# Performance work log

Measured on AMD Instinct MI355X. Metric: run time of the kernel, lower is better.

## Reference

```python
import jax, jax.numpy as jnp
import numpy as np

N, K, D = 65536, 1024, 512
ALPHA = 1.0

def setup_inputs() -> dict:
    key = jax.random.key(0)
    k1, k2 = jax.random.split(key)
    batch = jax.random.normal(k1, (N, D), dtype=jnp.float32)
    # Xavier uniform init for cluster centers: bound = sqrt(6/(K+D))
    bound = float(np.sqrt(6.0 / (K + D)))
    cluster_centers = jax.random.uniform(k2, (K, D), dtype=jnp.float32, minval=-bound, maxval=bound)
    return {"batch": batch, "cluster_centers": cluster_centers}

def reference(batch, cluster_centers):
    x_sq = jnp.sum(batch * batch, axis=1, keepdims=True)            # [N,1]
    c_sq = jnp.sum(cluster_centers * cluster_centers, axis=1)       # [K]
    cross = batch @ cluster_centers.T                               # [N,K]
    norm_squared = jnp.maximum(x_sq - 2.0 * cross + c_sq[None, :], 0.0)
    numerator = 1.0 / (1.0 + norm_squared / ALPHA)
    power = (ALPHA + 1.0) / 2.0
    numerator = numerator ** power
    return numerator / jnp.sum(numerator, axis=1, keepdims=True)
```

## Files before the change

kernel.cpp:

```cpp
#include <hip/hip_runtime.h>
#include <hip/hip_bf16.h>
#include <stdint.h>


#define N_ROWS 65536
#define K_CL   1024
#define D_DIM  512
#define BM     64

typedef __attribute__((ext_vector_type(8))) short short8;
typedef __attribute__((ext_vector_type(4))) float f32x4;

__device__ __forceinline__ ushort f2bf(float f) {
    union { float f; uint32_t u; } v; v.f = f;
    uint32_t u = v.u;
    u += 0x7fffu + ((u >> 16) & 1u);
    return (ushort)(u >> 16);
}

__device__ __forceinline__ float waveReduceSum(float s) {
#pragma unroll
    for (int off = 32; off; off >>= 1) s += __shfl_down(s, off, 64);
    return s;
}

__global__ void prep_rows(const float* __restrict__ X, ushort* __restrict__ Xbf,
                          float* __restrict__ sq) {
    const int row  = blockIdx.x * 4 + (threadIdx.x >> 6);
    const int lane = threadIdx.x & 63;
    const float4* src = (const float4*)(X + (size_t)row * D_DIM);
    float4 a = src[lane * 2];
    float4 b = src[lane * 2 + 1];
    float s = (a.x*a.x + a.y*a.y) + (a.z*a.z + a.w*a.w)
            + (b.x*b.x + b.y*b.y) + (b.z*b.z + b.w*b.w);
    uint4 o;
    o.x = (uint32_t)f2bf(a.x) | ((uint32_t)f2bf(a.y) << 16);
    o.y = (uint32_t)f2bf(a.z) | ((uint32_t)f2bf(a.w) << 16);
    o.z = (uint32_t)f2bf(b.x) | ((uint32_t)f2bf(b.y) << 16);
    o.w = (uint32_t)f2bf(b.z) | ((uint32_t)f2bf(b.w) << 16);
    *(uint4*)(Xbf + (size_t)row * D_DIM + lane * 8) = o;
    s = waveReduceSum(s);
    if (lane == 0) sq[row] = s;
}

__global__ __launch_bounds__(512, 2) void gemm_fused(
    const ushort* __restrict__ A, const ushort* __restrict__ B,
    const float* __restrict__ xsq, const float* __restrict__ csq,
    float* __restrict__ out)
{
    __shared__ __align__(16) ushort smA[2][BM * 64];

    const int tid  = threadIdx.x;
    const int w    = tid >> 6;
    const int lane = tid & 63;
    const int l4 = lane >> 4, l16 = lane & 15;
    const int rbase = blockIdx.x * BM;

    const int srow  = tid >> 3;
    const int sslot = (tid & 7) ^ (srow & 7);
    const ushort* gA = A + (size_t)(rbase + srow) * D_DIM + sslot * 8;
    ushort* ldsA[2] = { &smA[0][0] + w * 512, &smA[1][0] + w * 512 };

    const ushort* gB[8];
#pragma unroll
    for (int n = 0; n < 8; ++n)
        gB[n] = B + (size_t)(w * 128 + n * 16 + l16) * D_DIM + l4 * 8;

    f32x4 acc[4][8] = {};
    const int swz = (l16 & 7) << 4;

    __builtin_amdgcn_global_load_lds(
        (const __attribute__((address_space(1))) void*)gA,
        (__attribute__((address_space(3))) void*)ldsA[0], 16, 0, 0);
    __syncthreads();

#pragma unroll
    for (int s = 0; s < 16; ++s) {
        const int kt  = s * 32;
        const int buf = (s >> 1) & 1;

        short8 bf[8];
#pragma unroll
        for (int n = 0; n < 8; ++n)
            bf[n] = *(const short8*)(gB[n] + kt);

        if ((s & 1) == 0 && s < 14)
            __builtin_amdgcn_global_load_lds(
                (const __attribute__((address_space(1))) void*)(gA + kt + 64),
                (__attribute__((address_space(3))) void*)ldsA[buf ^ 1], 16, 0, 0);

        short8 af[4];
        const int cb = (s & 1) * 64;
#pragma unroll
        for (int m = 0; m < 4; ++m) {
            const int row = m * 16 + l16;
            af[m] = *(const short8*)((const char*)&smA[buf][0]
                    + row * 128 + ((cb + l4 * 16) ^ swz));
        }

        __builtin_amdgcn_s_setprio(1);
#pragma unroll
        for (int m = 0; m < 4; ++m)
#pragma unroll
            for (int n = 0; n < 8; ++n)
                acc[m][n] = __builtin_amdgcn_mfma_f32_16x16x32_bf16(
                    af[m], bf[n], acc[m][n], 0, 0, 0);
        __builtin_amdgcn_s_setprio(0);

        if (s & 1) __syncthreads();
    }

    float xs[4][4];
#pragma unroll
    for (int m = 0; m < 4; ++m)
#pragma unroll
        for (int r = 0; r < 4; ++r)
            xs[m][r] = xsq[rbase + m * 16 + l4 * 4 + r];

    float s[4][4] = {{0.f}};
#pragma unroll
    for (int n = 0; n < 8; ++n) {
        const float cs = csq[w * 128 + n * 16 + l16];
#pragma unroll
        for (int m = 0; m < 4; ++m)
#pragma unroll
            for (int r = 0; r < 4; ++r) {
                float ns = fmaxf(xs[m][r] - 2.0f * acc[m][n][r] + cs, 0.0f);
                float p = 1.0f / (1.0f + ns);
                acc[m][n][r] = p;
                s[m][r] += p;
            }
    }
#pragma unroll
    for (int m = 0; m < 4; ++m)
#pragma unroll
        for (int r = 0; r < 4; ++r) {
            float v = s[m][r];
            v += __shfl_xor(v, 1, 64);
            v += __shfl_xor(v, 2, 64);
            v += __shfl_xor(v, 4, 64);
            v += __shfl_xor(v, 8, 64);
            s[m][r] = v;
        }
    float* smRS  = (float*)&smA[0][0];
    float* smInv = (float*)&smA[0][0] + 512;
    if (l16 == 0) {
#pragma unroll
        for (int m = 0; m < 4; ++m)
#pragma unroll
            for (int r = 0; r < 4; ++r)
                smRS[w * 64 + m * 16 + l4 * 4 + r] = s[m][r];
    }
    __syncthreads();
    if (tid < 64) {
        float t = 0.f;
#pragma unroll
        for (int j = 0; j < 8; ++j) t += smRS[j * 64 + tid];
        smInv[tid] = 1.0f / t;
    }
    __syncthreads();

    float inv[4][4];
#pragma unroll
    for (int m = 0; m < 4; ++m)
#pragma unroll
        for (int r = 0; r < 4; ++r)
            inv[m][r] = smInv[m * 16 + l4 * 4 + r];

#pragma unroll
    for (int m = 0; m < 4; ++m)
#pragma unroll
        for (int n = 0; n < 8; ++n) {
            const int col = w * 128 + n * 16 + l16;
#pragma unroll
            for (int r = 0; r < 4; ++r) {
                const int row = rbase + m * 16 + l4 * 4 + r;
                out[(size_t)row * K_CL + col] = acc[m][n][r] * inv[m][r];
            }
        }
}

extern "C" void kernel_launch(void* const* d_in, const int* in_sizes, int n_in,
                              void* d_out, int out_size, void* d_ws, size_t ws_size,
                              hipStream_t stream) {
    const float* batch   = (const float*)d_in[0];
    const float* centers = (const float*)d_in[1];
    float* out = (float*)d_out;

    char* ws = (char*)d_ws;
    ushort* Abf = (ushort*)ws;
    ushort* Bbf = (ushort*)(ws + (size_t)N_ROWS * D_DIM * 2);
    float*  xsq = (float*)(ws + (size_t)N_ROWS * D_DIM * 2
                              + (size_t)K_CL * D_DIM * 2);
    float*  csq = xsq + N_ROWS;
    (void)in_sizes; (void)n_in; (void)out_size; (void)ws_size;

    prep_rows<<<K_CL / 4,   256, 0, stream>>>(centers, Bbf, csq);
    prep_rows<<<N_ROWS / 4, 256, 0, stream>>>(batch, Abf, xsq);
    gemm_fused<<<N_ROWS / BM, 512, 0, stream>>>(Abf, Bbf, xsq, csq, out);
}
```

Baseline: 253.0 us.

## Stage both A and B tiles through LDS with double-buffered async loads

B fragments were previously read straight from global memory into registers each k-step. Now both the A and B tiles, in BK=32 slices, are staged into double-buffered LDS with direct global-to-LDS loads and a swizzled layout. Explicit vmcnt waits and barriers overlap the next stage's loads with the current MFMAs. This removes exposed global load latency on B, at the cost of about 130KB of LDS per block, which likely limits occupancy to one block per CU despite launch_bounds(512,2).

```diff
diff --git a/kernel.cpp b/kernel.cpp
--- a/kernel.cpp
+++ b/kernel.cpp
@@ -7,6 +7,7 @@
 #define K_CL   1024
 #define D_DIM  512
 #define BM     64
+#define BK     32
 
 typedef __attribute__((ext_vector_type(8))) short short8;
 typedef __attribute__((ext_vector_type(4))) float f32x4;
@@ -48,7 +49,8 @@
     const float* __restrict__ xsq, const float* __restrict__ csq,
     float* __restrict__ out)
 {
-    __shared__ __align__(16) ushort smA[2][BM * 64];
+    __shared__ __align__(16) ushort smA[2][BM * BK];
+    __shared__ __align__(16) ushort smB[2][K_CL * BK];
 
     const int tid  = threadIdx.x;
     const int w    = tid >> 6;
@@ -56,47 +58,57 @@
     const int l4 = lane >> 4, l16 = lane & 15;
     const int rbase = blockIdx.x * BM;
 
-    const int srow  = tid >> 3;
-    const int sslot = (tid & 7) ^ (srow & 7);
-    const ushort* gA = A + (size_t)(rbase + srow) * D_DIM + sslot * 8;
-    ushort* ldsA[2] = { &smA[0][0] + w * 512, &smA[1][0] + w * 512 };
-
-    const ushort* gB[8];
-#pragma unroll
-    for (int n = 0; n < 8; ++n)
-        gB[n] = B + (size_t)(w * 128 + n * 16 + l16) * D_DIM + l4 * 8;
+    const int gslot = (tid & 3) ^ ((tid >> 3) & 3);
+    const int grow  = tid >> 2;
+    const ushort* srcA = A + (size_t)(rbase + grow) * D_DIM + gslot * 8;
+    const ushort* srcB = B + (size_t)grow * D_DIM + gslot * 8;
+
+    const int swz  = ((l16 >> 1) & 3) << 4;
+    const int aoff = l16 * 64 + ((l4 * 16) ^ swz);
+    const int boff = (w * 128 + l16) * 64 + ((l4 * 16) ^ swz);
 
     f32x4 acc[4][8] = {};
-    const int swz = (l16 & 7) << 4;
-
-    __builtin_amdgcn_global_load_lds(
-        (const __attribute__((address_space(1))) void*)gA,
-        (__attribute__((address_space(3))) void*)ldsA[0], 16, 0, 0);
-    __syncthreads();
-
-#pragma unroll
-    for (int s = 0; s < 16; ++s) {
-        const int kt  = s * 32;
-        const int buf = (s >> 1) & 1;
-
-        short8 bf[8];
+
+#define STAGE(sbuf, kt) do {                                                 \
+        if (w < 4)                                                           \
+            __builtin_amdgcn_global_load_lds(                                \
+                (const __attribute__((address_space(1))) void*)(srcA + (kt)),\
+                (__attribute__((address_space(3))) void*)(&smA[sbuf][0] + w * 512), \
+                16, 0, 0);                                                   \
+        _Pragma("unroll")                                                    \
+        for (int c = 0; c < 8; ++c)                                          \
+            __builtin_amdgcn_global_load_lds(                                \
+                (const __attribute__((address_space(1))) void*)(srcB + (size_t)c * 128 * D_DIM + (kt)), \
+                (__attribute__((address_space(3))) void*)(&smB[sbuf][0] + c * 4096 + w * 512), \
+                16, 0, 0);                                                   \
+    } while (0)
+
+    STAGE(0, 0);
+
+    for (int t = 0; t < 16; ++t) {
+        const int buf = t & 1;
+        __builtin_amdgcn_sched_barrier(0);
+        __builtin_amdgcn_s_barrier();
+        __builtin_amdgcn_sched_barrier(0);
+        if (t < 15) {
+            STAGE(buf ^ 1, (t + 1) * BK);
+            if (w < 4) asm volatile("s_waitcnt vmcnt(9)" ::: "memory");
+            else       asm volatile("s_waitcnt vmcnt(8)" ::: "memory");
+        } else {
+            asm volatile("s_waitcnt vmcnt(0)" ::: "memory");
+        }
+        __builtin_amdgcn_s_barrier();
+        __builtin_amdgcn_sched_barrier(0);
+
+        const char* bA = (const char*)&smA[buf][0];
+        const char* bB = (const char*)&smB[buf][0];
+        short8 af[4], bf[8];
+#pragma unroll
+        for (int m = 0; m < 4; ++m)
+            af[m] = *(const short8*)(bA + m * 1024 + aoff);
 #pragma unroll
         for (int n = 0; n < 8; ++n)
-            bf[n] = *(const short8*)(gB[n] + kt);
-
-        if ((s & 1) == 0 && s < 14)
-            __builtin_amdgcn_global_load_lds(
-                (const __attribute__((address_space(1))) void*)(gA + kt + 64),
-                (__attribute__((address_space(3))) void*)ldsA[buf ^ 1], 16, 0, 0);
-
-        short8 af[4];
-        const int cb = (s & 1) * 64;
-#pragma unroll
-        for (int m = 0; m < 4; ++m) {
-            const int row = m * 16 + l16;
-            af[m] = *(const short8*)((const char*)&smA[buf][0]
-                    + row * 128 + ((cb + l4 * 16) ^ swz));
-        }
+            bf[n] = *(const short8*)(bB + n * 1024 + boff);
 
         __builtin_amdgcn_s_setprio(1);
 #pragma unroll
@@ -106,9 +118,10 @@
                 acc[m][n] = __builtin_amdgcn_mfma_f32_16x16x32_bf16(
                     af[m], bf[n], acc[m][n], 0, 0, 0);
         __builtin_amdgcn_s_setprio(0);
-
-        if (s & 1) __syncthreads();
-    }
+    }
+#undef STAGE
+
+    __syncthreads();
 
     float xs[4][4];
 #pragma unroll
```

Result: faster. 228.9 us (-9.6%).

## Double row tile with 16 waves and load full A tile into LDS upfront

Applied to the files above, without the earlier changes.

Raises the row tile to 128 rows per block with 1024 threads arranged as 2x8 waves, so each B fragment loaded from global memory serves twice as many rows. The A tile (128x512 bf16, 128KB) is now loaded into LDS in one shot with an XOR swizzle, replacing the double-buffered streaming loop and its per-step barriers. This cuts B traffic and synchronization, but the 128KB LDS footprint and 1024-thread blocks likely limit occupancy to one block per CU, and no A load overlaps with compute.

```diff
diff --git a/kernel.cpp b/kernel.cpp
--- a/kernel.cpp
+++ b/kernel.cpp
@@ -6,7 +6,7 @@
 #define N_ROWS 65536
 #define K_CL   1024
 #define D_DIM  512
-#define BM     64
+#define BM     128
 
 typedef __attribute__((ext_vector_type(8))) short short8;
 typedef __attribute__((ext_vector_type(4))) float f32x4;
@@ -43,71 +43,62 @@
     if (lane == 0) sq[row] = s;
 }
 
-__global__ __launch_bounds__(512, 2) void gemm_fused(
+__global__ __launch_bounds__(1024, 2) void gemm_fused(
     const ushort* __restrict__ A, const ushort* __restrict__ B,
     const float* __restrict__ xsq, const float* __restrict__ csq,
     float* __restrict__ out)
 {
-    __shared__ __align__(16) ushort smA[2][BM * 64];
+    __shared__ __align__(16) ushort smA[BM * D_DIM];
 
     const int tid  = threadIdx.x;
     const int w    = tid >> 6;
     const int lane = tid & 63;
     const int l4 = lane >> 4, l16 = lane & 15;
+    const int wr = w >> 3, wc = w & 7;
     const int rbase = blockIdx.x * BM;
 
-    const int srow  = tid >> 3;
-    const int sslot = (tid & 7) ^ (srow & 7);
-    const ushort* gA = A + (size_t)(rbase + srow) * D_DIM + sslot * 8;
-    ushort* ldsA[2] = { &smA[0][0] + w * 512, &smA[1][0] + w * 512 };
+#pragma unroll
+    for (int i = 0; i < 8; ++i) {
+        const int row = i * 16 + w;
+        const int sl  = lane ^ (row & 15);
+        __builtin_amdgcn_global_load_lds(
+            (const __attribute__((address_space(1))) void*)
+                (A + (size_t)(rbase + row) * D_DIM + sl * 8),
+            (__attribute__((address_space(3))) void*)(smA + (size_t)row * D_DIM),
+            16, 0, 0);
+    }
 
     const ushort* gB[8];
 #pragma unroll
     for (int n = 0; n < 8; ++n)
-        gB[n] = B + (size_t)(w * 128 + n * 16 + l16) * D_DIM + l4 * 8;
+        gB[n] = B + (size_t)(wc * 128 + n * 16 + l16) * D_DIM + l4 * 8;
+
+    int abase[4];
+#pragma unroll
+    for (int m = 0; m < 4; ++m)
+        abase[m] = (wr * 64 + m * 16 + l16) * 1024;
 
     f32x4 acc[4][8] = {};
-    const int swz = (l16 & 7) << 4;
 
-    __builtin_amdgcn_global_load_lds(
-        (const __attribute__((address_space(1))) void*)gA,
-        (__attribute__((address_space(3))) void*)ldsA[0], 16, 0, 0);
     __syncthreads();
 
-#pragma unroll
-    for (int s = 0; s < 16; ++s) {
-        const int kt  = s * 32;
-        const int buf = (s >> 1) & 1;
-
+#pragma unroll 4
+    for (int t = 0; t < 16; ++t) {
         short8 bf[8];
 #pragma unroll
         for (int n = 0; n < 8; ++n)
-            bf[n] = *(const short8*)(gB[n] + kt);
-
-        if ((s & 1) == 0 && s < 14)
-            __builtin_amdgcn_global_load_lds(
-                (const __attribute__((address_space(1))) void*)(gA + kt + 64),
-                (__attribute__((address_space(3))) void*)ldsA[buf ^ 1], 16, 0, 0);
-
+            bf[n] = *(const short8*)(gB[n] + t * 32);
         short8 af[4];
-        const int cb = (s & 1) * 64;
 #pragma unroll
-        for (int m = 0; m < 4; ++m) {
-            const int row = m * 16 + l16;
-            af[m] = *(const short8*)((const char*)&smA[buf][0]
-                    + row * 128 + ((cb + l4 * 16) ^ swz));
-        }
-
-        __builtin_amdgcn_s_setprio(1);
+        for (int m = 0; m < 4; ++m)
+            af[m] = *(const short8*)((const char*)smA
+                    + abase[m] + ((((t * 4 + l4) ^ l16)) << 4));
 #pragma unroll
         for (int m = 0; m < 4; ++m)
 #pragma unroll
             for (int n = 0; n < 8; ++n)
                 acc[m][n] = __builtin_amdgcn_mfma_f32_16x16x32_bf16(
                     af[m], bf[n], acc[m][n], 0, 0, 0);
-        __builtin_amdgcn_s_setprio(0);
-
-        if (s & 1) __syncthreads();
     }
 
     float xs[4][4];
@@ -115,12 +106,12 @@
     for (int m = 0; m < 4; ++m)
 #pragma unroll
         for (int r = 0; r < 4; ++r)
-            xs[m][r] = xsq[rbase + m * 16 + l4 * 4 + r];
+            xs[m][r] = xsq[rbase + wr * 64 + m * 16 + l4 * 4 + r];
 
     float s[4][4] = {{0.f}};
 #pragma unroll
     for (int n = 0; n < 8; ++n) {
-        const float cs = csq[w * 128 + n * 16 + l16];
+        const float cs = csq[wc * 128 + n * 16 + l16];
 #pragma unroll
         for (int m = 0; m < 4; ++m)
 #pragma unroll
@@ -142,20 +133,22 @@
             v += __shfl_xor(v, 8, 64);
             s[m][r] = v;
         }
-    float* smRS  = (float*)&smA[0][0];
-    float* smInv = (float*)&smA[0][0] + 512;
+
+    __syncthreads();
+    float* smRS  = (float*)smA;
+    float* smInv = (float*)smA + 1024;
     if (l16 == 0) {
 #pragma unroll
         for (int m = 0; m < 4; ++m)
 #pragma unroll
             for (int r = 0; r < 4; ++r)
-                smRS[w * 64 + m * 16 + l4 * 4 + r] = s[m][r];
+                smRS[wc * 128 + wr * 64 + m * 16 + l4 * 4 + r] = s[m][r];
     }
     __syncthreads();
-    if (tid < 64) {
+    if (tid < 128) {
         float t = 0.f;
 #pragma unroll
-        for (int j = 0; j < 8; ++j) t += smRS[j * 64 + tid];
+        for (int j = 0; j < 8; ++j) t += smRS[j * 128 + tid];
         smInv[tid] = 1.0f / t;
     }
     __syncthreads();
@@ -165,16 +158,16 @@
     for (int m = 0; m < 4; ++m)
 #pragma unroll
         for (int r = 0; r < 4; ++r)
-            inv[m][r] = smInv[m * 16 + l4 * 4 + r];
+            inv[m][r] = smInv[wr * 64 + m * 16 + l4 * 4 + r];
 
 #pragma unroll
     for (int m = 0; m < 4; ++m)
 #pragma unroll
         for (int n = 0; n < 8; ++n) {
-            const int col = w * 128 + n * 16 + l16;
+            const int col = wc * 128 + n * 16 + l16;
 #pragma unroll
             for (int r = 0; r < 4; ++r) {
-                const int row = rbase + m * 16 + l4 * 4 + r;
+                const int row = rbase + wr * 64 + m * 16 + l4 * 4 + r;
                 out[(size_t)row * K_CL + col] = acc[m][n][r] * inv[m][r];
             }
         }
@@ -197,5 +190,5 @@
 
     prep_rows<<<K_CL / 4,   256, 0, stream>>>(centers, Bbf, csq);
     prep_rows<<<N_ROWS / 4, 256, 0, stream>>>(batch, Abf, xsq);
-    gemm_fused<<<N_ROWS / BM, 512, 0, stream>>>(Abf, Bbf, xsq, csq, out);
+    gemm_fused<<<N_ROWS / BM, 1024, 0, stream>>>(Abf, Bbf, xsq, csq, out);
 }
```

New measurement: 1.009 ms. 299% more time.
